# Kernel optimization log

Hardware: AMD Instinct MI355X
Metric: run time of the kernel (lower is better)

The kernel has to match this reference:

```python
import jax, jax.numpy as jnp
import numpy as np

N_NODES = 100000
N_EDGES = 625000
D_IN = 128
D_HID = 256


def setup_inputs() -> dict:
    key = jax.random.key(0)
    ks = jax.random.split(key, 8)
    x = jax.random.normal(ks[0], (N_NODES, D_IN), dtype=jnp.float32)
    edge_index = jax.random.randint(ks[1], (2, N_EDGES), 0, N_NODES, dtype=jnp.int64)
    s_in = 1.0 / np.sqrt(D_IN)
    s_hid = 1.0 / np.sqrt(D_HID)
    # SAGEConv layer 0: lin_l (on aggregated neighbors, with bias) and lin_r (root)
    W_l0 = jax.random.uniform(ks[2], (D_IN, D_HID), jnp.float32, -s_in, s_in)
    W_r0 = jax.random.uniform(ks[3], (D_IN, D_HID), jnp.float32, -s_in, s_in)
    b0 = jnp.zeros((D_HID,), jnp.float32)
    # SAGEConv layer 1
    W_l1 = jax.random.uniform(ks[4], (D_HID, D_HID), jnp.float32, -s_hid, s_hid)
    W_r1 = jax.random.uniform(ks[5], (D_HID, D_HID), jnp.float32, -s_hid, s_hid)
    b1 = jnp.zeros((D_HID,), jnp.float32)
    return {"x": x, "edge_index": edge_index,
            "W_l0": W_l0, "W_r0": W_r0, "b0": b0,
            "W_l1": W_l1, "W_r1": W_r1, "b1": b1}


def _sage_conv(x, src, dst, W_l, W_r, b):
    """PyG SAGEConv with mean aggregation: lin_l(mean_{j in N(i)} x_j) + lin_r(x_i)."""
    n = x.shape[0]
    msg = x[src]  # [E, d] gather of source-node features
    agg_sum = jax.ops.segment_sum(msg, dst, num_segments=n)  # scatter-add to targets
    cnt = jax.ops.segment_sum(jnp.ones_like(dst, dtype=x.dtype), dst, num_segments=n)
    agg = agg_sum / jnp.maximum(cnt, 1.0)[:, None]  # mean over neighbors
    return agg @ W_l + b + x @ W_r


def reference(x, edge_index, W_l0, W_r0, b0, W_l1, W_r1, b1):
    src, dst = edge_index[0], edge_index[1]
    h = _sage_conv(x, src, dst, W_l0, W_r0, b0)
    h = jax.nn.relu(h)  # dropout is identity at inference
    h = _sage_conv(h, src, dst, W_l1, W_r1, b1)
    h = jax.nn.relu(h)
    return h
```

## Files before the change

kernel.cpp:

```cpp
#include <hip/hip_runtime.h>


constexpr int NN   = 100000;
constexpr int NE   = 625000;
constexpr int DIN  = 128;
constexpr int DHID = 256;
constexpr int NB   = (NN + 255) / 256;
constexpr int CONV_BLKS = NN * DIN / 8 / 256;

using short8 = __attribute__((ext_vector_type(8))) short;
using f32x4  = __attribute__((ext_vector_type(4))) float;

__device__ __forceinline__ float bf2f(unsigned int u) {
    return __uint_as_float(u << 16);
}
__device__ __forceinline__ unsigned short f2b(float f) {
    unsigned int u = __float_as_uint(f);
    unsigned int r = (u + 0x7fffu + ((u >> 16) & 1u)) >> 16;
    return (unsigned short)r;
}
__device__ __forceinline__ unsigned int pack2(float lo, float hi) {
    return (unsigned int)f2b(lo) | ((unsigned int)f2b(hi) << 16);
}
__device__ __forceinline__ void gload16(const void* g, void* lds) {
    __builtin_amdgcn_global_load_lds(
        (const __attribute__((address_space(1))) void*)g,
        (__attribute__((address_space(3))) void*)lds, 16, 0, 0);
}

__global__ __launch_bounds__(256) void zero_kernel(int* __restrict__ p, int n)
{
    int t = blockIdx.x * 256 + threadIdx.x;
    if (t < n) p[t] = 0;
}

__global__ __launch_bounds__(256) void hist_kernel(const int* __restrict__ dst,
                                                   int* __restrict__ hist)
{
    int t = blockIdx.x * 256 + threadIdx.x;
    if (t < NE) atomicAdd(&hist[dst[t]], 1);
}

__global__ __launch_bounds__(256) void chunk_sum_kernel(const int* __restrict__ hist,
                                                        int* __restrict__ bsum)
{
    __shared__ int s[256];
    int i = blockIdx.x * 256 + threadIdx.x;
    s[threadIdx.x] = (i < NN) ? hist[i] : 0;
    __syncthreads();
    for (int off = 128; off > 0; off >>= 1) {
        if (threadIdx.x < off) s[threadIdx.x] += s[threadIdx.x + off];
        __syncthreads();
    }
    if (threadIdx.x == 0) bsum[blockIdx.x] = s[0];
}

__global__ __launch_bounds__(512) void scan_bsum_kernel(const int* __restrict__ bsum,
                                                        int* __restrict__ bpre)
{
    __shared__ int s[512];
    int t = threadIdx.x;
    int v = (t < NB) ? bsum[t] : 0;
    s[t] = v;
    __syncthreads();
    for (int off = 1; off < 512; off <<= 1) {
        int u = (t >= off) ? s[t - off] : 0;
        __syncthreads();
        s[t] += u;
        __syncthreads();
    }
    if (t < NB) bpre[t] = s[t] - v;
}

__global__ __launch_bounds__(256) void scatter_offs_kernel(const int* __restrict__ hist,
                                                           const int* __restrict__ bpre,
                                                           int* __restrict__ offs,
                                                           int* __restrict__ cursor)
{
    __shared__ int s[256];
    int t = threadIdx.x;
    int i = blockIdx.x * 256 + t;
    int v = (i < NN) ? hist[i] : 0;
    s[t] = v;
    __syncthreads();
    for (int off = 1; off < 256; off <<= 1) {
        int u = (t >= off) ? s[t - off] : 0;
        __syncthreads();
        s[t] += u;
        __syncthreads();
    }
    int excl = s[t] - v + bpre[blockIdx.x];
    if (i < NN) {
        offs[i]   = excl;
        cursor[i] = excl;
    }
    if (i == NN - 1) offs[NN] = NE;
}

__global__ __launch_bounds__(256) void perm_kernel(const int* __restrict__ src,
                                                   const int* __restrict__ dst,
                                                   int* __restrict__ cursor,
                                                   int* __restrict__ perm)
{
    int t = blockIdx.x * 256 + threadIdx.x;
    if (t < NE) {
        int p = atomicAdd(&cursor[dst[t]], 1);
        perm[p] = src[t];
    }
}

__global__ __launch_bounds__(256) void prep_all_kernel(
    const float* __restrict__ x, unsigned short* __restrict__ xb,
    const float* __restrict__ Wl0, const float* __restrict__ Wr0,
    unsigned short* __restrict__ WT0,
    const float* __restrict__ Wl1, const float* __restrict__ Wr1,
    unsigned short* __restrict__ WT1)
{
    int b = blockIdx.x;
    if (b < CONV_BLKS) {
        int t = b * 256 + threadIdx.x;
        float4 v0 = reinterpret_cast<const float4*>(x)[t * 2 + 0];
        float4 v1 = reinterpret_cast<const float4*>(x)[t * 2 + 1];
        uint4 o;
        o.x = pack2(v0.x, v0.y); o.y = pack2(v0.z, v0.w);
        o.z = pack2(v1.x, v1.y); o.w = pack2(v1.z, v1.w);
        reinterpret_cast<uint4*>(xb)[t] = o;
    } else if (b < CONV_BLKS + 256) {
        int t = (b - CONV_BLKS) * 256 + threadIdx.x;
        int n = t >> 8, k = t & 255;
        float v = (k < DIN) ? Wl0[(size_t)k * DHID + n]
                            : Wr0[(size_t)(k - DIN) * DHID + n];
        WT0[t] = f2b(v);
    } else {
        int t = (b - CONV_BLKS - 256) * 256 + threadIdx.x;
        int n = t >> 9, k = t & 511;
        float v = (k < DHID) ? Wl1[(size_t)k * DHID + n]
                             : Wr1[(size_t)(k - DHID) * DHID + n];
        WT1[t] = f2b(v);
    }
}

template <int D>
__global__ __launch_bounds__(256) void gather_mean_kernel(
    const int* __restrict__ offs, const int* __restrict__ perm,
    const unsigned short* __restrict__ feat, unsigned short* __restrict__ agg)
{
    const int w    = (blockIdx.x * 256 + threadIdx.x) >> 6;
    const int lane = threadIdx.x & 63;
    if (w >= NN) return;
    const int beg = offs[w], end = offs[w + 1];
    const int deg = end - beg;
    const float sc = 1.0f / (float)(deg > 1 ? deg : 1);

    if constexpr (D == 256) {
        const uint2* base = reinterpret_cast<const uint2*>(feat);
        float a0[4] = {}, a1[4] = {}, a2[4] = {}, a3[4] = {};
        for (int e0 = 0; e0 < deg; e0 += 64) {
            const int chunk = min(deg - e0, 64);
            int pv = (lane < chunk) ? perm[beg + e0 + lane] : 0;
            int i = chunk & 3;
            if (i > 0) {
                int s = __builtin_amdgcn_readlane(pv, 0);
                uint2 v = base[(size_t)s * 64 + lane];
                a1[0] += bf2f(v.x & 0xffffu); a1[1] += bf2f(v.x >> 16);
                a1[2] += bf2f(v.y & 0xffffu); a1[3] += bf2f(v.y >> 16);
            }
            if (i > 1) {
                int s = __builtin_amdgcn_readlane(pv, 1);
                uint2 v = base[(size_t)s * 64 + lane];
                a2[0] += bf2f(v.x & 0xffffu); a2[1] += bf2f(v.x >> 16);
                a2[2] += bf2f(v.y & 0xffffu); a2[3] += bf2f(v.y >> 16);
            }
            if (i > 2) {
                int s = __builtin_amdgcn_readlane(pv, 2);
                uint2 v = base[(size_t)s * 64 + lane];
                a3[0] += bf2f(v.x & 0xffffu); a3[1] += bf2f(v.x >> 16);
                a3[2] += bf2f(v.y & 0xffffu); a3[3] += bf2f(v.y >> 16);
            }
            for (; i + 4 <= chunk; i += 4) {
                int s0 = __builtin_amdgcn_readlane(pv, i + 0);
                int s1 = __builtin_amdgcn_readlane(pv, i + 1);
                int s2 = __builtin_amdgcn_readlane(pv, i + 2);
                int s3 = __builtin_amdgcn_readlane(pv, i + 3);
                uint2 v0 = base[(size_t)s0 * 64 + lane];
                uint2 v1 = base[(size_t)s1 * 64 + lane];
                uint2 v2 = base[(size_t)s2 * 64 + lane];
                uint2 v3 = base[(size_t)s3 * 64 + lane];
                a0[0] += bf2f(v0.x & 0xffffu); a0[1] += bf2f(v0.x >> 16);
                a0[2] += bf2f(v0.y & 0xffffu); a0[3] += bf2f(v0.y >> 16);
                a1[0] += bf2f(v1.x & 0xffffu); a1[1] += bf2f(v1.x >> 16);
                a1[2] += bf2f(v1.y & 0xffffu); a1[3] += bf2f(v1.y >> 16);
                a2[0] += bf2f(v2.x & 0xffffu); a2[1] += bf2f(v2.x >> 16);
                a2[2] += bf2f(v2.y & 0xffffu); a2[3] += bf2f(v2.y >> 16);
                a3[0] += bf2f(v3.x & 0xffffu); a3[1] += bf2f(v3.x >> 16);
                a3[2] += bf2f(v3.y & 0xffffu); a3[3] += bf2f(v3.y >> 16);
            }
        }
        float r0 = (a0[0] + a1[0]) + (a2[0] + a3[0]);
        float r1 = (a0[1] + a1[1]) + (a2[1] + a3[1]);
        float r2 = (a0[2] + a1[2]) + (a2[2] + a3[2]);
        float r3 = (a0[3] + a1[3]) + (a2[3] + a3[3]);
        uint2 o;
        o.x = pack2(r0 * sc, r1 * sc);
        o.y = pack2(r2 * sc, r3 * sc);
        reinterpret_cast<uint2*>(agg)[(size_t)w * 64 + lane] = o;
    } else {
        const unsigned int* base = reinterpret_cast<const unsigned int*>(feat);
        float a0[2] = {}, a1[2] = {}, a2[2] = {}, a3[2] = {};
        for (int e0 = 0; e0 < deg; e0 += 64) {
            const int chunk = min(deg - e0, 64);
            int pv = (lane < chunk) ? perm[beg + e0 + lane] : 0;
            int i = chunk & 3;
            if (i > 0) {
                int s = __builtin_amdgcn_readlane(pv, 0);
                unsigned int v = base[(size_t)s * 64 + lane];
                a1[0] += bf2f(v & 0xffffu); a1[1] += bf2f(v >> 16);
            }
            if (i > 1) {
                int s = __builtin_amdgcn_readlane(pv, 1);
                unsigned int v = base[(size_t)s * 64 + lane];
                a2[0] += bf2f(v & 0xffffu); a2[1] += bf2f(v >> 16);
            }
            if (i > 2) {
                int s = __builtin_amdgcn_readlane(pv, 2);
                unsigned int v = base[(size_t)s * 64 + lane];
                a3[0] += bf2f(v & 0xffffu); a3[1] += bf2f(v >> 16);
            }
            for (; i + 4 <= chunk; i += 4) {
                int s0 = __builtin_amdgcn_readlane(pv, i + 0);
                int s1 = __builtin_amdgcn_readlane(pv, i + 1);
                int s2 = __builtin_amdgcn_readlane(pv, i + 2);
                int s3 = __builtin_amdgcn_readlane(pv, i + 3);
                unsigned int v0 = base[(size_t)s0 * 64 + lane];
                unsigned int v1 = base[(size_t)s1 * 64 + lane];
                unsigned int v2 = base[(size_t)s2 * 64 + lane];
                unsigned int v3 = base[(size_t)s3 * 64 + lane];
                a0[0] += bf2f(v0 & 0xffffu); a0[1] += bf2f(v0 >> 16);
                a1[0] += bf2f(v1 & 0xffffu); a1[1] += bf2f(v1 >> 16);
                a2[0] += bf2f(v2 & 0xffffu); a2[1] += bf2f(v2 >> 16);
                a3[0] += bf2f(v3 & 0xffffu); a3[1] += bf2f(v3 >> 16);
            }
        }
        float r0 = (a0[0] + a1[0]) + (a2[0] + a3[0]);
        float r1 = (a0[1] + a1[1]) + (a2[1] + a3[1]);
        reinterpret_cast<unsigned int*>(agg)[(size_t)w * 64 + lane] = pack2(r0 * sc, r1 * sc);
    }
}

template <int KP, bool WF, bool WB>
__global__ __launch_bounds__(512) void sage_mfma_gemm(
    const unsigned short* __restrict__ Aagg,
    const unsigned short* __restrict__ Axr,
    const unsigned short* __restrict__ WT,
    const float* __restrict__ bias,
    float* __restrict__ outf,
    unsigned short* __restrict__ outb,
    int M)
{
    __shared__ __align__(16) unsigned short As[3 * 4096];
    __shared__ __align__(16) unsigned short Bs[3 * 8192];

    const int t   = threadIdx.x;
    const int l   = t & 63;
    const int wid = t >> 6;
    const int wr  = wid >> 2;
    const int wc  = wid & 3;
    const int m0  = blockIdx.x * 128;

    const int rin = l >> 2;
    const int csw = (l & 3) ^ ((l >> 3) & 3);

    const int sc0 = wid * 3, sc1 = sc0 + 1, sc2 = sc0 + 2;

    constexpr int K2 = 2 * KP;
    constexpr int KT = K2 / 32;

    auto stageChunk = [&](int buf, int kt, int ch) {
        const int kb = kt * 32;
        if (ch < 8) {
            const unsigned short* Asrc;
            int kk;
            if (kb < KP) { Asrc = Aagg; kk = kb; }
            else         { Asrc = Axr;  kk = kb - KP; }
            int row = m0 + ch * 16 + rin; if (row >= M) row = M - 1;
            gload16(Asrc + (size_t)row * KP + kk + csw * 8,
                    As + buf * 4096 + ch * 512);
        } else {
            int row = (ch - 8) * 16 + rin;
            gload16(WT + (size_t)row * K2 + kb + csw * 8,
                    Bs + buf * 8192 + (ch - 8) * 512);
        }
    };
    auto stage = [&](int buf, int kt) {
        stageChunk(buf, kt, sc0);
        stageChunk(buf, kt, sc1);
        stageChunk(buf, kt, sc2);
    };

    const int fr  = l & 15;
    const int swz = ((l >> 4) ^ ((l >> 1) & 3)) * 8;
    const int aOff = (wr * 64 + fr) * 32 + swz;
    const int bOff = (wc * 64 + fr) * 32 + swz;

    f32x4 acc[4][4] = {};

    stage(0, 0);
    stage(1, 1);

    int cur = 0;
    for (int kt = 0; kt < KT; ++kt) {
        if (kt + 2 < KT) {
            int nb = cur + 2; if (nb >= 3) nb -= 3;
            stage(nb, kt + 2);
            asm volatile("s_waitcnt vmcnt(6)" ::: "memory");
        } else if (kt + 1 < KT) {
            asm volatile("s_waitcnt vmcnt(3)" ::: "memory");
        } else {
            asm volatile("s_waitcnt vmcnt(0)" ::: "memory");
        }
        __builtin_amdgcn_s_barrier();
        __builtin_amdgcn_sched_barrier(0);

        const unsigned short* Ard = As + cur * 4096 + aOff;
        const unsigned short* Brd = Bs + cur * 8192 + bOff;
        short8 af[4], bf[4];
        #pragma unroll
        for (int i = 0; i < 4; ++i)
            af[i] = *reinterpret_cast<const short8*>(Ard + i * 512);
        #pragma unroll
        for (int i = 0; i < 4; ++i)
            bf[i] = *reinterpret_cast<const short8*>(Brd + i * 512);
        #pragma unroll
        for (int i = 0; i < 4; ++i)
            #pragma unroll
            for (int j = 0; j < 4; ++j)
                acc[i][j] = __builtin_amdgcn_mfma_f32_16x16x32_bf16(
                    af[i], bf[j], acc[i][j], 0, 0, 0);

        asm volatile("s_waitcnt lgkmcnt(0)" ::: "memory");
        __builtin_amdgcn_s_barrier();
        __builtin_amdgcn_sched_barrier(0);
        cur = (cur == 2) ? 0 : cur + 1;
    }

    const int rq = (l >> 4) * 4;
    #pragma unroll
    for (int fn = 0; fn < 4; ++fn) {
        const int col = wc * 64 + fn * 16 + fr;
        const float bb = bias[col];
        #pragma unroll
        for (int fm = 0; fm < 4; ++fm) {
            const int rbase = m0 + wr * 64 + fm * 16 + rq;
            #pragma unroll
            for (int j = 0; j < 4; ++j) {
                const int r = rbase + j;
                if (r < M) {
                    float v = fmaxf(acc[fm][fn][j] + bb, 0.f);
                    if (WF) outf[(size_t)r * DHID + col] = v;
                    if (WB) outb[(size_t)r * DHID + col] = f2b(v);
                }
            }
        }
    }
}

extern "C" void kernel_launch(void* const* d_in, const int* in_sizes, int n_in,
                              void* d_out, int out_size, void* d_ws, size_t ws_size,
                              hipStream_t stream)
{
    const float* x   = (const float*)d_in[0];
    const int*   ei  = (const int*)d_in[1];
    const int*   src = ei;
    const int*   dst = ei + NE;
    const float* Wl0 = (const float*)d_in[2];
    const float* Wr0 = (const float*)d_in[3];
    const float* b0  = (const float*)d_in[4];
    const float* Wl1 = (const float*)d_in[5];
    const float* Wr1 = (const float*)d_in[6];
    const float* b1  = (const float*)d_in[7];
    float* out = (float*)d_out;

    char* ws = (char*)d_ws;
    int*            hist   = (int*)(ws);
    int*            offs   = (int*)(ws + 400384);
    int*            perm   = (int*)(ws + 801024);
    int*            bsum   = (int*)(ws + 3301376);
    int*            bpre   = (int*)(ws + 3305472);
    int*            cursor = (int*)(ws + 3309568);
    unsigned short* WT0    = (unsigned short*)(ws + 3709952);
    unsigned short* WT1    = (unsigned short*)(ws + 3841024);
    unsigned short* xb     = (unsigned short*)(ws + 4103168);
    unsigned short* h0b    = (unsigned short*)(ws + 29703168);
    unsigned short* aggb   = (unsigned short*)(ws + 80903168);

    zero_kernel<<<(NN + 255) / 256, 256, 0, stream>>>(hist, NN);
    hist_kernel<<<(NE + 255) / 256, 256, 0, stream>>>(dst, hist);
    chunk_sum_kernel<<<NB, 256, 0, stream>>>(hist, bsum);
    scan_bsum_kernel<<<1, 512, 0, stream>>>(bsum, bpre);
    scatter_offs_kernel<<<NB, 256, 0, stream>>>(hist, bpre, offs, cursor);
    perm_kernel<<<(NE + 255) / 256, 256, 0, stream>>>(src, dst, cursor, perm);

    prep_all_kernel<<<CONV_BLKS + 256 + 512, 256, 0, stream>>>(
        x, xb, Wl0, Wr0, WT0, Wl1, Wr1, WT1);

    constexpr int NWBLK = (NN * 64) / 256;
    const int GEMM_BLKS = (NN + 127) / 128;

    gather_mean_kernel<DIN><<<NWBLK, 256, 0, stream>>>(offs, perm, xb, aggb);
    sage_mfma_gemm<DIN, false, true><<<GEMM_BLKS, 512, 0, stream>>>(
        aggb, xb, WT0, b0, nullptr, h0b, NN);

    gather_mean_kernel<DHID><<<NWBLK, 256, 0, stream>>>(offs, perm, h0b, aggb);
    sage_mfma_gemm<DHID, true, false><<<GEMM_BLKS, 512, 0, stream>>>(
        aggb, h0b, WT1, b1, out, nullptr, NN);
}
```

Measured before the change: 273.7 us.

## Widen gather loads to half-wave per edge, double-buffer GEMM, fold hist zeroing into prep

The gather-mean kernel now splits each wave into two halves that process different edges at once, using 16-byte (or 8-byte) loads per lane, and combines the halves with a cross-lane shuffle. This gives more memory parallelism and wider transactions per edge. Separately, the GEMM pipeline drops from triple to double buffering, which cuts LDS use and may raise occupancy but prefetches one tile ahead instead of two. The histogram zeroing is folded into the prep kernel to save one launch.

```diff
diff --git a/kernel.cpp b/kernel.cpp
--- a/kernel.cpp
+++ b/kernel.cpp
@@ -26,12 +26,6 @@
     __builtin_amdgcn_global_load_lds(
         (const __attribute__((address_space(1))) void*)g,
         (__attribute__((address_space(3))) void*)lds, 16, 0, 0);
-}
-
-__global__ __launch_bounds__(256) void zero_kernel(int* __restrict__ p, int n)
-{
-    int t = blockIdx.x * 256 + threadIdx.x;
-    if (t < n) p[t] = 0;
 }
 
 __global__ __launch_bounds__(256) void hist_kernel(const int* __restrict__ dst,
@@ -114,7 +108,8 @@
     const float* __restrict__ Wl0, const float* __restrict__ Wr0,
     unsigned short* __restrict__ WT0,
     const float* __restrict__ Wl1, const float* __restrict__ Wr1,
-    unsigned short* __restrict__ WT1)
+    unsigned short* __restrict__ WT1,
+    int* __restrict__ hist)
 {
     int b = blockIdx.x;
     if (b < CONV_BLKS) {
@@ -131,12 +126,15 @@
         float v = (k < DIN) ? Wl0[(size_t)k * DHID + n]
                             : Wr0[(size_t)(k - DIN) * DHID + n];
         WT0[t] = f2b(v);
-    } else {
+    } else if (b < CONV_BLKS + 256 + 512) {
         int t = (b - CONV_BLKS - 256) * 256 + threadIdx.x;
         int n = t >> 9, k = t & 511;
         float v = (k < DHID) ? Wl1[(size_t)k * DHID + n]
                              : Wr1[(size_t)(k - DHID) * DHID + n];
         WT1[t] = f2b(v);
+    } else {
+        int t = (b - CONV_BLKS - 256 - 512) * 256 + threadIdx.x;
+        if (t < NN) hist[t] = 0;
     }
 }
 
@@ -145,105 +143,90 @@
     const int* __restrict__ offs, const int* __restrict__ perm,
     const unsigned short* __restrict__ feat, unsigned short* __restrict__ agg)
 {
-    const int w    = (blockIdx.x * 256 + threadIdx.x) >> 6;
-    const int lane = threadIdx.x & 63;
+    const int w = (blockIdx.x * 256 + threadIdx.x) >> 6;
+    const int l = threadIdx.x & 63;
+    const int h = l >> 5;
+    const int c = l & 31;
     if (w >= NN) return;
     const int beg = offs[w], end = offs[w + 1];
     const int deg = end - beg;
     const float sc = 1.0f / (float)(deg > 1 ? deg : 1);
 
     if constexpr (D == 256) {
-        const uint2* base = reinterpret_cast<const uint2*>(feat);
-        float a0[4] = {}, a1[4] = {}, a2[4] = {}, a3[4] = {};
+        const uint4* base = reinterpret_cast<const uint4*>(feat);
+        float A0[8] = {}, A1[8] = {};
         for (int e0 = 0; e0 < deg; e0 += 64) {
             const int chunk = min(deg - e0, 64);
-            int pv = (lane < chunk) ? perm[beg + e0 + lane] : 0;
-            int i = chunk & 3;
-            if (i > 0) {
-                int s = __builtin_amdgcn_readlane(pv, 0);
-                uint2 v = base[(size_t)s * 64 + lane];
-                a1[0] += bf2f(v.x & 0xffffu); a1[1] += bf2f(v.x >> 16);
-                a1[2] += bf2f(v.y & 0xffffu); a1[3] += bf2f(v.y >> 16);
-            }
-            if (i > 1) {
-                int s = __builtin_amdgcn_readlane(pv, 1);
-                uint2 v = base[(size_t)s * 64 + lane];
-                a2[0] += bf2f(v.x & 0xffffu); a2[1] += bf2f(v.x >> 16);
-                a2[2] += bf2f(v.y & 0xffffu); a2[3] += bf2f(v.y >> 16);
-            }
-            if (i > 2) {
-                int s = __builtin_amdgcn_readlane(pv, 2);
-                uint2 v = base[(size_t)s * 64 + lane];
-                a3[0] += bf2f(v.x & 0xffffu); a3[1] += bf2f(v.x >> 16);
-                a3[2] += bf2f(v.y & 0xffffu); a3[3] += bf2f(v.y >> 16);
-            }
-            for (; i + 4 <= chunk; i += 4) {
-                int s0 = __builtin_amdgcn_readlane(pv, i + 0);
-                int s1 = __builtin_amdgcn_readlane(pv, i + 1);
-                int s2 = __builtin_amdgcn_readlane(pv, i + 2);
-                int s3 = __builtin_amdgcn_readlane(pv, i + 3);
-                uint2 v0 = base[(size_t)s0 * 64 + lane];
-                uint2 v1 = base[(size_t)s1 * 64 + lane];
-                uint2 v2 = base[(size_t)s2 * 64 + lane];
-                uint2 v3 = base[(size_t)s3 * 64 + lane];
-                a0[0] += bf2f(v0.x & 0xffffu); a0[1] += bf2f(v0.x >> 16);
-                a0[2] += bf2f(v0.y & 0xffffu); a0[3] += bf2f(v0.y >> 16);
-                a1[0] += bf2f(v1.x & 0xffffu); a1[1] += bf2f(v1.x >> 16);
-                a1[2] += bf2f(v1.y & 0xffffu); a1[3] += bf2f(v1.y >> 16);
-                a2[0] += bf2f(v2.x & 0xffffu); a2[1] += bf2f(v2.x >> 16);
-                a2[2] += bf2f(v2.y & 0xffffu); a2[3] += bf2f(v2.y >> 16);
-                a3[0] += bf2f(v3.x & 0xffffu); a3[1] += bf2f(v3.x >> 16);
-                a3[2] += bf2f(v3.y & 0xffffu); a3[3] += bf2f(v3.y >> 16);
-            }
-        }
-        float r0 = (a0[0] + a1[0]) + (a2[0] + a3[0]);
-        float r1 = (a0[1] + a1[1]) + (a2[1] + a3[1]);
-        float r2 = (a0[2] + a1[2]) + (a2[2] + a3[2]);
-        float r3 = (a0[3] + a1[3]) + (a2[3] + a3[3]);
-        uint2 o;
-        o.x = pack2(r0 * sc, r1 * sc);
-        o.y = pack2(r2 * sc, r3 * sc);
-        reinterpret_cast<uint2*>(agg)[(size_t)w * 64 + lane] = o;
+            int pv = (l < chunk) ? perm[beg + e0 + l] : 0;
+            auto dopair = [&](float* A, int p) {
+                int sA = __builtin_amdgcn_readlane(pv, 2 * p);
+                int sB = __builtin_amdgcn_readlane(pv, 2 * p + 1);
+                int e  = 2 * p + h;
+                int s  = h ? sB : sA;
+                float m = (e < chunk) ? 1.0f : 0.0f;
+                uint4 v = base[(size_t)s * 32 + c];
+                A[0] = fmaf(bf2f(v.x & 0xffffu), m, A[0]);
+                A[1] = fmaf(bf2f(v.x >> 16),     m, A[1]);
+                A[2] = fmaf(bf2f(v.y & 0xffffu), m, A[2]);
+                A[3] = fmaf(bf2f(v.y >> 16),     m, A[3]);
+                A[4] = fmaf(bf2f(v.z & 0xffffu), m, A[4]);
+                A[5] = fmaf(bf2f(v.z >> 16),     m, A[5]);
+                A[6] = fmaf(bf2f(v.w & 0xffffu), m, A[6]);
+                A[7] = fmaf(bf2f(v.w >> 16),     m, A[7]);
+            };
+            const int np = (chunk + 1) >> 1;
+            int p = 0;
+            if (np & 1) { dopair(A1, 0); p = 1; }
+            for (; p < np; p += 2) { dopair(A0, p); dopair(A1, p + 1); }
+        }
+        float r[8];
+        #pragma unroll
+        for (int j = 0; j < 8; ++j) {
+            r[j] = A0[j] + A1[j];
+            r[j] += __shfl_xor(r[j], 32);
+            r[j] *= sc;
+        }
+        if (l < 32) {
+            uint4 o;
+            o.x = pack2(r[0], r[1]); o.y = pack2(r[2], r[3]);
+            o.z = pack2(r[4], r[5]); o.w = pack2(r[6], r[7]);
+            reinterpret_cast<uint4*>(agg)[(size_t)w * 32 + c] = o;
+        }
     } else {
-        const unsigned int* base = reinterpret_cast<const unsigned int*>(feat);
-        float a0[2] = {}, a1[2] = {}, a2[2] = {}, a3[2] = {};
+        const uint2* base = reinterpret_cast<const uint2*>(feat);
+        float A0[4] = {}, A1[4] = {};
         for (int e0 = 0; e0 < deg; e0 += 64) {
             const int chunk = min(deg - e0, 64);
-            int pv = (lane < chunk) ? perm[beg + e0 + lane] : 0;
-            int i = chunk & 3;
-            if (i > 0) {
-                int s = __builtin_amdgcn_readlane(pv, 0);
-                unsigned int v = base[(size_t)s * 64 + lane];
-                a1[0] += bf2f(v & 0xffffu); a1[1] += bf2f(v >> 16);
-            }
-            if (i > 1) {
-                int s = __builtin_amdgcn_readlane(pv, 1);
-                unsigned int v = base[(size_t)s * 64 + lane];
-                a2[0] += bf2f(v & 0xffffu); a2[1] += bf2f(v >> 16);
-            }
-            if (i > 2) {
-                int s = __builtin_amdgcn_readlane(pv, 2);
-                unsigned int v = base[(size_t)s * 64 + lane];
-                a3[0] += bf2f(v & 0xffffu); a3[1] += bf2f(v >> 16);
-            }
-            for (; i + 4 <= chunk; i += 4) {
-                int s0 = __builtin_amdgcn_readlane(pv, i + 0);
-                int s1 = __builtin_amdgcn_readlane(pv, i + 1);
-                int s2 = __builtin_amdgcn_readlane(pv, i + 2);
-                int s3 = __builtin_amdgcn_readlane(pv, i + 3);
-                unsigned int v0 = base[(size_t)s0 * 64 + lane];
-                unsigned int v1 = base[(size_t)s1 * 64 + lane];
-                unsigned int v2 = base[(size_t)s2 * 64 + lane];
-                unsigned int v3 = base[(size_t)s3 * 64 + lane];
-                a0[0] += bf2f(v0 & 0xffffu); a0[1] += bf2f(v0 >> 16);
-                a1[0] += bf2f(v1 & 0xffffu); a1[1] += bf2f(v1 >> 16);
-                a2[0] += bf2f(v2 & 0xffffu); a2[1] += bf2f(v2 >> 16);
-                a3[0] += bf2f(v3 & 0xffffu); a3[1] += bf2f(v3 >> 16);
-            }
-        }
-        float r0 = (a0[0] + a1[0]) + (a2[0] + a3[0]);
-        float r1 = (a0[1] + a1[1]) + (a2[1] + a3[1]);
-        reinterpret_cast<unsigned int*>(agg)[(size_t)w * 64 + lane] = pack2(r0 * sc, r1 * sc);
+            int pv = (l < chunk) ? perm[beg + e0 + l] : 0;
+            auto dopair = [&](float* A, int p) {
+                int sA = __builtin_amdgcn_readlane(pv, 2 * p);
+                int sB = __builtin_amdgcn_readlane(pv, 2 * p + 1);
+                int e  = 2 * p + h;
+                int s  = h ? sB : sA;
+                float m = (e < chunk) ? 1.0f : 0.0f;
+                uint2 v = base[(size_t)s * 32 + c];
+                A[0] = fmaf(bf2f(v.x & 0xffffu), m, A[0]);
+                A[1] = fmaf(bf2f(v.x >> 16),     m, A[1]);
+                A[2] = fmaf(bf2f(v.y & 0xffffu), m, A[2]);
+                A[3] = fmaf(bf2f(v.y >> 16),     m, A[3]);
+            };
+            const int np = (chunk + 1) >> 1;
+            int p = 0;
+            if (np & 1) { dopair(A1, 0); p = 1; }
+            for (; p < np; p += 2) { dopair(A0, p); dopair(A1, p + 1); }
+        }
+        float r[4];
+        #pragma unroll
+        for (int j = 0; j < 4; ++j) {
+            r[j] = A0[j] + A1[j];
+            r[j] += __shfl_xor(r[j], 32);
+            r[j] *= sc;
+        }
+        if (l < 32) {
+            uint2 o;
+            o.x = pack2(r[0], r[1]); o.y = pack2(r[2], r[3]);
+            reinterpret_cast<uint2*>(agg)[(size_t)w * 32 + c] = o;
+        }
     }
 }
 
@@ -257,8 +240,8 @@
     unsigned short* __restrict__ outb,
     int M)
 {
-    __shared__ __align__(16) unsigned short As[3 * 4096];
-    __shared__ __align__(16) unsigned short Bs[3 * 8192];
+    __shared__ __align__(16) unsigned short As[2 * 4096];
+    __shared__ __align__(16) unsigned short Bs[2 * 8192];
 
     const int t   = threadIdx.x;
     const int l   = t & 63;
@@ -305,15 +288,11 @@
     f32x4 acc[4][4] = {};
 
     stage(0, 0);
-    stage(1, 1);
 
     int cur = 0;
     for (int kt = 0; kt < KT; ++kt) {
-        if (kt + 2 < KT) {
-            int nb = cur + 2; if (nb >= 3) nb -= 3;
-            stage(nb, kt + 2);
-            asm volatile("s_waitcnt vmcnt(6)" ::: "memory");
-        } else if (kt + 1 < KT) {
+        if (kt + 1 < KT) {
+            stage(cur ^ 1, kt + 1);
             asm volatile("s_waitcnt vmcnt(3)" ::: "memory");
         } else {
             asm volatile("s_waitcnt vmcnt(0)" ::: "memory");
@@ -340,7 +319,7 @@
         asm volatile("s_waitcnt lgkmcnt(0)" ::: "memory");
         __builtin_amdgcn_s_barrier();
         __builtin_amdgcn_sched_barrier(0);
-        cur = (cur == 2) ? 0 : cur + 1;
+        cur ^= 1;
     }
 
     const int rq = (l >> 4) * 4;
@@ -393,16 +372,14 @@
     unsigned short* h0b    = (unsigned short*)(ws + 29703168);
     unsigned short* aggb   = (unsigned short*)(ws + 80903168);
 
-    zero_kernel<<<(NN + 255) / 256, 256, 0, stream>>>(hist, NN);
+    prep_all_kernel<<<CONV_BLKS + 256 + 512 + NB, 256, 0, stream>>>(
+        x, xb, Wl0, Wr0, WT0, Wl1, Wr1, WT1, hist);
     hist_kernel<<<(NE + 255) / 256, 256, 0, stream>>>(dst, hist);
     chunk_sum_kernel<<<NB, 256, 0, stream>>>(hist, bsum);
     scan_bsum_kernel<<<1, 512, 0, stream>>>(bsum, bpre);
     scatter_offs_kernel<<<NB, 256, 0, stream>>>(hist, bpre, offs, cursor);
     perm_kernel<<<(NE + 255) / 256, 256, 0, stream>>>(src, dst, cursor, perm);
 
-    prep_all_kernel<<<CONV_BLKS + 256 + 512, 256, 0, stream>>>(
-        x, xb, Wl0, Wr0, WT0, Wl1, Wr1, WT1);
-
     constexpr int NWBLK = (NN * 64) / 256;
     const int GEMM_BLKS = (NN + 127) / 128;
 
```

After: 269.7 us. About the same (-1.5%).
